# Kernel optimization log

Measured on AMD Instinct MI355X. Metric: run time of the kernel, lower is better.

Reference implementation:

```python
import jax, jax.numpy as jnp
import numpy as np

EPS = 1e-07

def setup_inputs() -> dict:
    key = jax.random.key(0)
    k1, k2, k3, k4 = jax.random.split(key, 4)
    B, IN, OUT = 8192, 2048, 2048
    input_tensor = jax.random.normal(k1, (B, IN), dtype=jnp.float32)
    # truncated_normal(stddev=0.02) init approximated with scaled normal
    W_hat = 0.02 * jax.random.normal(k2, (IN, OUT), dtype=jnp.float32)
    M_hat = 0.02 * jax.random.normal(k3, (IN, OUT), dtype=jnp.float32)
    gate = 0.02 * jax.random.normal(k4, (IN, OUT), dtype=jnp.float32)
    return {"input_tensor": input_tensor, "W_hat": W_hat, "M_hat": M_hat, "gate": gate}

def reference(input_tensor, W_hat, M_hat, gate):
    W = jnp.tanh(W_hat) * jax.nn.sigmoid(M_hat)          # [IN, OUT]
    a = input_tensor @ W                                  # additive path [B, OUT]
    m = jnp.exp(jnp.log(jnp.abs(input_tensor) + EPS) @ W) # multiplicative path [B, OUT]
    g = jax.nn.sigmoid(input_tensor @ gate)               # gate [B, OUT]
    return g * a + (1.0 - g) * m
```

## Files before the change

### kernel.cpp

```cpp
#include <hip/hip_runtime.h>
#include <stdint.h>

typedef __attribute__((ext_vector_type(8))) short short8;
typedef __attribute__((ext_vector_type(4))) float floatx4;

#define B_DIM 8192
#define K_DIM 2048
#define N_DIM 2048

__device__ __forceinline__ unsigned short f2bf(float f) {
    union { float f; unsigned u; } v; v.f = f;
    unsigned r = v.u + 0x7fffu + ((v.u >> 16) & 1u);
    return (unsigned short)(r >> 16);
}

__device__ __forceinline__ void gld_lds16(const void* g, void* l) {
    __builtin_amdgcn_global_load_lds(
        (const __attribute__((address_space(1))) void*)g,
        (__attribute__((address_space(3))) void*)l, 16, 0, 0);
}

__global__ __launch_bounds__(256) void prep_x(const float4* __restrict__ X4,
                                              ushort* __restrict__ Xb,
                                              ushort* __restrict__ Lb) {
    int i = blockIdx.x * 256 + threadIdx.x;
    float4 v = X4[i];
    ushort4 xb, lb;
    xb.x = f2bf(v.x); xb.y = f2bf(v.y); xb.z = f2bf(v.z); xb.w = f2bf(v.w);
    lb.x = f2bf(__logf(fabsf(v.x) + 1e-7f));
    lb.y = f2bf(__logf(fabsf(v.y) + 1e-7f));
    lb.z = f2bf(__logf(fabsf(v.z) + 1e-7f));
    lb.w = f2bf(__logf(fabsf(v.w) + 1e-7f));
    *(ushort4*)(Xb + (size_t)i * 4) = xb;
    *(ushort4*)(Lb + (size_t)i * 4) = lb;
}

__global__ __launch_bounds__(256) void prep_wg(const float* __restrict__ Wh,
                                               const float* __restrict__ Mh,
                                               const float* __restrict__ Gf,
                                               ushort* __restrict__ Wt,
                                               ushort* __restrict__ Gt) {
    __shared__ float tw[32][33];
    __shared__ float tg[32][33];
    const int k0 = blockIdx.y * 32, n0 = blockIdx.x * 32;
    const int tx = threadIdx.x, ty = threadIdx.y;
#pragma unroll
    for (int i = 0; i < 4; i++) {
        int k = k0 + ty + i * 8;
        int n = n0 + tx;
        size_t idx = (size_t)k * N_DIM + n;
        float wh = Wh[idx], mh = Mh[idx];
        tw[ty + i * 8][tx] = tanhf(wh) * (1.f / (1.f + __expf(-mh)));
        tg[ty + i * 8][tx] = Gf[idx];
    }
    __syncthreads();
#pragma unroll
    for (int i = 0; i < 4; i++) {
        int n = n0 + ty + i * 8;
        int k = k0 + tx;
        Wt[(size_t)n * K_DIM + k] = f2bf(tw[tx][ty + i * 8]);
        Gt[(size_t)n * K_DIM + k] = f2bf(tg[tx][ty + i * 8]);
    }
}

__global__ __launch_bounds__(256, 2) void gemm_g(const ushort* __restrict__ Xb,
                                                 const ushort* __restrict__ Gt,
                                                 float* __restrict__ out) {
    __shared__ ushort sA[128 * 32];
    __shared__ ushort sB[128 * 32];
    const int t = threadIdx.x;
    const int lane = t & 63;
    const int w = t >> 6;
    const int wm = w >> 1, wn = w & 1;
    const int rowA = blockIdx.y * 128;
    const int rowB = blockIdx.x * 128;

    floatx4 acc[4][4];
    const floatx4 z = {0.f, 0.f, 0.f, 0.f};
#pragma unroll
    for (int i = 0; i < 4; i++)
#pragma unroll
        for (int j = 0; j < 4; j++) acc[i][j] = z;

    const int r0 = t >> 2;
    const int c8 = (t & 3) << 3;
    const ushort* gA0 = Xb + (size_t)(rowA + r0) * K_DIM + c8;
    const ushort* gA1 = gA0 + (size_t)64 * K_DIM;
    const ushort* gB0 = Gt + (size_t)(rowB + r0) * K_DIM + c8;
    const ushort* gB1 = gB0 + (size_t)64 * K_DIM;
    ushort* lA0 = sA + t * 8;
    ushort* lA1 = sA + (t + 256) * 8;
    ushort* lB0 = sB + t * 8;
    ushort* lB1 = sB + (t + 256) * 8;

    const int lr = lane & 15;
    const int lk = (lane >> 4) << 3;

    for (int k0 = 0; k0 < K_DIM; k0 += 32) {
        gld_lds16(gA0 + k0, lA0);
        gld_lds16(gA1 + k0, lA1);
        gld_lds16(gB0 + k0, lB0);
        gld_lds16(gB1 + k0, lB1);
        asm volatile("s_waitcnt vmcnt(0)" ::: "memory");
        __syncthreads();
        short8 af[4], bf[4];
#pragma unroll
        for (int mi = 0; mi < 4; mi++)
            af[mi] = *(const short8*)(sA + (wm * 64 + mi * 16 + lr) * 32 + lk);
#pragma unroll
        for (int ni = 0; ni < 4; ni++)
            bf[ni] = *(const short8*)(sB + (wn * 64 + ni * 16 + lr) * 32 + lk);
#pragma unroll
        for (int ni = 0; ni < 4; ni++)
#pragma unroll
            for (int mi = 0; mi < 4; mi++)
                acc[mi][ni] = __builtin_amdgcn_mfma_f32_16x16x32_bf16(af[mi], bf[ni], acc[mi][ni], 0, 0, 0);
        __syncthreads();
    }

    const int rsub = (lane >> 4) << 2;
#pragma unroll
    for (int mi = 0; mi < 4; mi++)
#pragma unroll
        for (int ni = 0; ni < 4; ni++)
#pragma unroll
            for (int r = 0; r < 4; r++) {
                int row = rowA + wm * 64 + mi * 16 + rsub + r;
                int col = rowB + wn * 64 + ni * 16 + lr;
                float v = acc[mi][ni][r];
                out[(size_t)row * N_DIM + col] = 1.f / (1.f + __expf(-v));
            }
}

__global__ __launch_bounds__(256, 2) void gemm_am(const ushort* __restrict__ Xb,
                                                  const ushort* __restrict__ Lb,
                                                  const ushort* __restrict__ Wt,
                                                  float* __restrict__ out) {
    __shared__ ushort sA[128 * 32];
    __shared__ ushort sL[128 * 32];
    __shared__ ushort sB[128 * 32];
    const int t = threadIdx.x;
    const int lane = t & 63;
    const int w = t >> 6;
    const int wm = w >> 1, wn = w & 1;
    const int rowA = blockIdx.y * 128;
    const int rowB = blockIdx.x * 128;

    floatx4 acca[4][4], accm[4][4];
    const floatx4 z = {0.f, 0.f, 0.f, 0.f};
#pragma unroll
    for (int i = 0; i < 4; i++)
#pragma unroll
        for (int j = 0; j < 4; j++) { acca[i][j] = z; accm[i][j] = z; }

    const int r0 = t >> 2;
    const int c8 = (t & 3) << 3;
    const ushort* gA0 = Xb + (size_t)(rowA + r0) * K_DIM + c8;
    const ushort* gA1 = gA0 + (size_t)64 * K_DIM;
    const ushort* gL0 = Lb + (size_t)(rowA + r0) * K_DIM + c8;
    const ushort* gL1 = gL0 + (size_t)64 * K_DIM;
    const ushort* gB0 = Wt + (size_t)(rowB + r0) * K_DIM + c8;
    const ushort* gB1 = gB0 + (size_t)64 * K_DIM;
    ushort* lA0 = sA + t * 8;
    ushort* lA1 = sA + (t + 256) * 8;
    ushort* lL0 = sL + t * 8;
    ushort* lL1 = sL + (t + 256) * 8;
    ushort* lB0 = sB + t * 8;
    ushort* lB1 = sB + (t + 256) * 8;

    const int lr = lane & 15;
    const int lk = (lane >> 4) << 3;

    for (int k0 = 0; k0 < K_DIM; k0 += 32) {
        gld_lds16(gA0 + k0, lA0);
        gld_lds16(gA1 + k0, lA1);
        gld_lds16(gL0 + k0, lL0);
        gld_lds16(gL1 + k0, lL1);
        gld_lds16(gB0 + k0, lB0);
        gld_lds16(gB1 + k0, lB1);
        asm volatile("s_waitcnt vmcnt(0)" ::: "memory");
        __syncthreads();
        short8 bw[4];
#pragma unroll
        for (int ni = 0; ni < 4; ni++)
            bw[ni] = *(const short8*)(sB + (wn * 64 + ni * 16 + lr) * 32 + lk);
#pragma unroll
        for (int mi = 0; mi < 4; mi++) {
            short8 ax = *(const short8*)(sA + (wm * 64 + mi * 16 + lr) * 32 + lk);
            short8 al = *(const short8*)(sL + (wm * 64 + mi * 16 + lr) * 32 + lk);
#pragma unroll
            for (int ni = 0; ni < 4; ni++) {
                acca[mi][ni] = __builtin_amdgcn_mfma_f32_16x16x32_bf16(ax, bw[ni], acca[mi][ni], 0, 0, 0);
                accm[mi][ni] = __builtin_amdgcn_mfma_f32_16x16x32_bf16(al, bw[ni], accm[mi][ni], 0, 0, 0);
            }
        }
        __syncthreads();
    }

    const int rsub = (lane >> 4) << 2;
#pragma unroll
    for (int mi = 0; mi < 4; mi++)
#pragma unroll
        for (int ni = 0; ni < 4; ni++)
#pragma unroll
            for (int r = 0; r < 4; r++) {
                int row = rowA + wm * 64 + mi * 16 + rsub + r;
                int col = rowB + wn * 64 + ni * 16 + lr;
                size_t idx = (size_t)row * N_DIM + col;
                float g = out[idx];
                float a = acca[mi][ni][r];
                float m = __expf(accm[mi][ni][r]);
                out[idx] = g * a + (1.f - g) * m;
            }
}

extern "C" void kernel_launch(void* const* d_in, const int* in_sizes, int n_in,
                              void* d_out, int out_size, void* d_ws, size_t ws_size,
                              hipStream_t stream) {
    const float* X  = (const float*)d_in[0];
    const float* Wh = (const float*)d_in[1];
    const float* Mh = (const float*)d_in[2];
    const float* Gf = (const float*)d_in[3];
    float* out = (float*)d_out;

    char* ws = (char*)d_ws;
    ushort* Xb = (ushort*)(ws);
    ushort* Lb = (ushort*)(ws + (size_t)B_DIM * K_DIM * 2);
    ushort* Wt = (ushort*)(ws + (size_t)B_DIM * K_DIM * 4);
    ushort* Gt = (ushort*)(ws + (size_t)B_DIM * K_DIM * 4 + (size_t)N_DIM * K_DIM * 2);

    prep_x<<<dim3((B_DIM * K_DIM) / (256 * 4)), dim3(256), 0, stream>>>(
        (const float4*)X, Xb, Lb);

    prep_wg<<<dim3(N_DIM / 32, K_DIM / 32), dim3(32, 8), 0, stream>>>(Wh, Mh, Gf, Wt, Gt);

    gemm_g<<<dim3(N_DIM / 128, B_DIM / 128), dim3(256), 0, stream>>>(Xb, Gt, out);

    gemm_am<<<dim3(N_DIM / 128, B_DIM / 128), dim3(256), 0, stream>>>(Xb, Lb, Wt, out);
}
```

Before: 402.7 us.

## Fuse gate GEMM into additive/multiplicative GEMM kernel

Merges the separate gate GEMM and the additive/multiplicative GEMM into one kernel that computes three accumulators per tile, sharing the X tile loads and computing the sigmoid in registers. This removes the fp32 gate write and read-back through global memory, one kernel launch, and the second read of Xb. In exchange it needs 48 accumulator vectors per thread and more LDS, and launch bounds drop to one block per SM, which lowers occupancy and latency hiding.

```diff
diff --git a/kernel.cpp b/kernel.cpp
--- a/kernel.cpp
+++ b/kernel.cpp
@@ -63,11 +63,15 @@
     }
 }
 
-__global__ __launch_bounds__(256, 2) void gemm_g(const ushort* __restrict__ Xb,
-                                                 const ushort* __restrict__ Gt,
-                                                 float* __restrict__ out) {
-    __shared__ ushort sA[128 * 32];
-    __shared__ ushort sB[128 * 32];
+__global__ __launch_bounds__(256, 1) void gemm_fused(const ushort* __restrict__ Xb,
+                                                     const ushort* __restrict__ Lb,
+                                                     const ushort* __restrict__ Wt,
+                                                     const ushort* __restrict__ Gt,
+                                                     float* __restrict__ out) {
+    __shared__ ushort sX[128 * 32];
+    __shared__ ushort sL[128 * 32];
+    __shared__ ushort sW[128 * 32];
+    __shared__ ushort sG[128 * 32];
     const int t = threadIdx.x;
     const int lane = t & 63;
     const int w = t >> 6;
@@ -75,123 +79,61 @@
     const int rowA = blockIdx.y * 128;
     const int rowB = blockIdx.x * 128;
 
-    floatx4 acc[4][4];
+    floatx4 acca[4][4], accm[4][4], accg[4][4];
     const floatx4 z = {0.f, 0.f, 0.f, 0.f};
 #pragma unroll
     for (int i = 0; i < 4; i++)
 #pragma unroll
-        for (int j = 0; j < 4; j++) acc[i][j] = z;
+        for (int j = 0; j < 4; j++) { acca[i][j] = z; accm[i][j] = z; accg[i][j] = z; }
 
     const int r0 = t >> 2;
     const int c8 = (t & 3) << 3;
-    const ushort* gA0 = Xb + (size_t)(rowA + r0) * K_DIM + c8;
-    const ushort* gA1 = gA0 + (size_t)64 * K_DIM;
-    const ushort* gB0 = Gt + (size_t)(rowB + r0) * K_DIM + c8;
-    const ushort* gB1 = gB0 + (size_t)64 * K_DIM;
-    ushort* lA0 = sA + t * 8;
-    ushort* lA1 = sA + (t + 256) * 8;
-    ushort* lB0 = sB + t * 8;
-    ushort* lB1 = sB + (t + 256) * 8;
+    const ushort* gX0 = Xb + (size_t)(rowA + r0) * K_DIM + c8;
+    const ushort* gX1 = gX0 + (size_t)64 * K_DIM;
+    const ushort* gL0 = Lb + (size_t)(rowA + r0) * K_DIM + c8;
+    const ushort* gL1 = gL0 + (size_t)64 * K_DIM;
+    const ushort* gW0 = Wt + (size_t)(rowB + r0) * K_DIM + c8;
+    const ushort* gW1 = gW0 + (size_t)64 * K_DIM;
+    const ushort* gG0 = Gt + (size_t)(rowB + r0) * K_DIM + c8;
+    const ushort* gG1 = gG0 + (size_t)64 * K_DIM;
+    ushort* lX0 = sX + t * 8;
+    ushort* lX1 = sX + (t + 256) * 8;
+    ushort* lL0 = sL + t * 8;
+    ushort* lL1 = sL + (t + 256) * 8;
+    ushort* lW0 = sW + t * 8;
+    ushort* lW1 = sW + (t + 256) * 8;
+    ushort* lG0 = sG + t * 8;
+    ushort* lG1 = sG + (t + 256) * 8;
 
     const int lr = lane & 15;
     const int lk = (lane >> 4) << 3;
 
     for (int k0 = 0; k0 < K_DIM; k0 += 32) {
-        gld_lds16(gA0 + k0, lA0);
-        gld_lds16(gA1 + k0, lA1);
-        gld_lds16(gB0 + k0, lB0);
-        gld_lds16(gB1 + k0, lB1);
+        gld_lds16(gX0 + k0, lX0);
+        gld_lds16(gX1 + k0, lX1);
+        gld_lds16(gL0 + k0, lL0);
+        gld_lds16(gL1 + k0, lL1);
+        gld_lds16(gW0 + k0, lW0);
+        gld_lds16(gW1 + k0, lW1);
+        gld_lds16(gG0 + k0, lG0);
+        gld_lds16(gG1 + k0, lG1);
         asm volatile("s_waitcnt vmcnt(0)" ::: "memory");
         __syncthreads();
-        short8 af[4], bf[4];
+        short8 bw[4], bg[4];
 #pragma unroll
-        for (int mi = 0; mi < 4; mi++)
-            af[mi] = *(const short8*)(sA + (wm * 64 + mi * 16 + lr) * 32 + lk);
-#pragma unroll
-        for (int ni = 0; ni < 4; ni++)
-            bf[ni] = *(const short8*)(sB + (wn * 64 + ni * 16 + lr) * 32 + lk);
-#pragma unroll
-        for (int ni = 0; ni < 4; ni++)
-#pragma unroll
-            for (int mi = 0; mi < 4; mi++)
-                acc[mi][ni] = __builtin_amdgcn_mfma_f32_16x16x32_bf16(af[mi], bf[ni], acc[mi][ni], 0, 0, 0);
-        __syncthreads();
-    }
-
-    const int rsub = (lane >> 4) << 2;
-#pragma unroll
-    for (int mi = 0; mi < 4; mi++)
-#pragma unroll
-        for (int ni = 0; ni < 4; ni++)
-#pragma unroll
-            for (int r = 0; r < 4; r++) {
-                int row = rowA + wm * 64 + mi * 16 + rsub + r;
-                int col = rowB + wn * 64 + ni * 16 + lr;
-                float v = acc[mi][ni][r];
-                out[(size_t)row * N_DIM + col] = 1.f / (1.f + __expf(-v));
-            }
-}
-
-__global__ __launch_bounds__(256, 2) void gemm_am(const ushort* __restrict__ Xb,
-                                                  const ushort* __restrict__ Lb,
-                                                  const ushort* __restrict__ Wt,
-                                                  float* __restrict__ out) {
-    __shared__ ushort sA[128 * 32];
-    __shared__ ushort sL[128 * 32];
-    __shared__ ushort sB[128 * 32];
-    const int t = threadIdx.x;
-    const int lane = t & 63;
-    const int w = t >> 6;
-    const int wm = w >> 1, wn = w & 1;
-    const int rowA = blockIdx.y * 128;
-    const int rowB = blockIdx.x * 128;
-
-    floatx4 acca[4][4], accm[4][4];
-    const floatx4 z = {0.f, 0.f, 0.f, 0.f};
-#pragma unroll
-    for (int i = 0; i < 4; i++)
-#pragma unroll
-        for (int j = 0; j < 4; j++) { acca[i][j] = z; accm[i][j] = z; }
-
-    const int r0 = t >> 2;
-    const int c8 = (t & 3) << 3;
-    const ushort* gA0 = Xb + (size_t)(rowA + r0) * K_DIM + c8;
-    const ushort* gA1 = gA0 + (size_t)64 * K_DIM;
-    const ushort* gL0 = Lb + (size_t)(rowA + r0) * K_DIM + c8;
-    const ushort* gL1 = gL0 + (size_t)64 * K_DIM;
-    const ushort* gB0 = Wt + (size_t)(rowB + r0) * K_DIM + c8;
-    const ushort* gB1 = gB0 + (size_t)64 * K_DIM;
-    ushort* lA0 = sA + t * 8;
-    ushort* lA1 = sA + (t + 256) * 8;
-    ushort* lL0 = sL + t * 8;
-    ushort* lL1 = sL + (t + 256) * 8;
-    ushort* lB0 = sB + t * 8;
-    ushort* lB1 = sB + (t + 256) * 8;
-
-    const int lr = lane & 15;
-    const int lk = (lane >> 4) << 3;
-
-    for (int k0 = 0; k0 < K_DIM; k0 += 32) {
-        gld_lds16(gA0 + k0, lA0);
-        gld_lds16(gA1 + k0, lA1);
-        gld_lds16(gL0 + k0, lL0);
-        gld_lds16(gL1 + k0, lL1);
-        gld_lds16(gB0 + k0, lB0);
-        gld_lds16(gB1 + k0, lB1);
-        asm volatile("s_waitcnt vmcnt(0)" ::: "memory");
-        __syncthreads();
-        short8 bw[4];
-#pragma unroll
-        for (int ni = 0; ni < 4; ni++)
-            bw[ni] = *(const short8*)(sB + (wn * 64 + ni * 16 + lr) * 32 + lk);
+        for (int ni = 0; ni < 4; ni++) {
+            bw[ni] = *(const short8*)(sW + (wn * 64 + ni * 16 + lr) * 32 + lk);
+            bg[ni] = *(const short8*)(sG + (wn * 64 + ni * 16 + lr) * 32 + lk);
+        }
 #pragma unroll
         for (int mi = 0; mi < 4; mi++) {
-            short8 ax = *(const short8*)(sA + (wm * 64 + mi * 16 + lr) * 32 + lk);
+            short8 ax = *(const short8*)(sX + (wm * 64 + mi * 16 + lr) * 32 + lk);
             short8 al = *(const short8*)(sL + (wm * 64 + mi * 16 + lr) * 32 + lk);
 #pragma unroll
             for (int ni = 0; ni < 4; ni++) {
                 acca[mi][ni] = __builtin_amdgcn_mfma_f32_16x16x32_bf16(ax, bw[ni], acca[mi][ni], 0, 0, 0);
                 accm[mi][ni] = __builtin_amdgcn_mfma_f32_16x16x32_bf16(al, bw[ni], accm[mi][ni], 0, 0, 0);
+                accg[mi][ni] = __builtin_amdgcn_mfma_f32_16x16x32_bf16(ax, bg[ni], accg[mi][ni], 0, 0, 0);
             }
         }
         __syncthreads();
@@ -206,11 +148,10 @@
             for (int r = 0; r < 4; r++) {
                 int row = rowA + wm * 64 + mi * 16 + rsub + r;
                 int col = rowB + wn * 64 + ni * 16 + lr;
-                size_t idx = (size_t)row * N_DIM + col;
-                float g = out[idx];
+                float g = 1.f / (1.f + __expf(-accg[mi][ni][r]));
                 float a = acca[mi][ni][r];
                 float m = __expf(accm[mi][ni][r]);
-                out[idx] = g * a + (1.f - g) * m;
+                out[(size_t)row * N_DIM + col] = g * a + (1.f - g) * m;
             }
 }
 
@@ -234,7 +175,5 @@
 
     prep_wg<<<dim3(N_DIM / 32, K_DIM / 32), dim3(32, 8), 0, stream>>>(Wh, Mh, Gf, Wt, Gt);
 
-    gemm_g<<<dim3(N_DIM / 128, B_DIM / 128), dim3(256), 0, stream>>>(Xb, Gt, out);
-
-    gemm_am<<<dim3(N_DIM / 128, B_DIM / 128), dim3(256), 0, stream>>>(Xb, Lb, Wt, out);
+    gemm_fused<<<dim3(N_DIM / 128, B_DIM / 128), dim3(256), 0, stream>>>(Xb, Lb, Wt, Gt, out);
 }
```

Result: slower. 517.2 us (+28.4%).
